# Optimization experiments

Measured on AMD Instinct MI355X. Metric: run time of the kernel, lower is better.

## Reference

```python
import jax, jax.numpy as jnp
import numpy as np

V_MIN = -10.0
V_MAX = 10.0
N_ATOMS = 101
LN_EPS = 1e-5

B = 131072
N_OBS = 60
N_ACT = 20
H = 256


def _layer_norm(x, g, b):
    mu = jnp.mean(x, axis=-1, keepdims=True)
    var = jnp.mean(jnp.square(x - mu), axis=-1, keepdims=True)
    return (x - mu) * jax.lax.rsqrt(var + LN_EPS) * g + b


def _mlp(x, W1, b1, g1, be1, W2, b2, g2, be2, W3, b3, g3, be3, W4, b4):
    h = jax.nn.silu(_layer_norm(x @ W1 + b1, g1, be1))
    h = jax.nn.silu(_layer_norm(h @ W2 + b2, g2, be2))
    h = jax.nn.silu(_layer_norm(h @ W3 + b3, g3, be3))
    return h @ W4 + b4  # [B, N_ATOMS] logits


def setup_inputs() -> dict:
    key = jax.random.key(0)
    ks = jax.random.split(key, 10)
    s = 0.05
    return {
        'obs': jax.random.normal(ks[0], (B, N_OBS), jnp.float32),
        'actions': jax.random.normal(ks[1], (B, N_ACT), jnp.float32),
        'rewards': jax.random.normal(ks[2], (B,), jnp.float32),
        'bootstrap': jax.random.uniform(ks[3], (B,), jnp.float32),
        'discount': jax.random.uniform(ks[4], (B,), jnp.float32, 0.95, 0.99),
        'q_support': jnp.linspace(V_MIN, V_MAX, N_ATOMS, dtype=jnp.float32),
        'W1': jax.random.normal(ks[5], (N_OBS + N_ACT, H), jnp.float32) * s,
        'b1': jnp.zeros((H,), jnp.float32),
        'g1': jnp.ones((H,), jnp.float32),
        'be1': jnp.zeros((H,), jnp.float32),
        'W2': jax.random.normal(ks[6], (H, H // 2), jnp.float32) * s,
        'b2': jnp.zeros((H // 2,), jnp.float32),
        'g2': jnp.ones((H // 2,), jnp.float32),
        'be2': jnp.zeros((H // 2,), jnp.float32),
        'W3': jax.random.normal(ks[7], (H // 2, H // 4), jnp.float32) * s,
        'b3': jnp.zeros((H // 4,), jnp.float32),
        'g3': jnp.ones((H // 4,), jnp.float32),
        'be3': jnp.zeros((H // 4,), jnp.float32),
        'W4': jax.random.normal(ks[8], (H // 4, N_ATOMS), jnp.float32) * s,
        'b4': jnp.zeros((N_ATOMS,), jnp.float32),
    }


def reference(obs, actions, rewards, bootstrap, discount, q_support,
              W1, b1, g1, be1, W2, b2, g2, be2, W3, b3, g3, be3, W4, b4):
    batch = rewards.shape[0]
    delta_z = (V_MAX - V_MIN) / (N_ATOMS - 1)
    # Bellman target support: [B, N_ATOMS]
    target_z = rewards[:, None] + bootstrap[:, None] * discount[:, None] * q_support
    target_z = jnp.clip(target_z, V_MIN, V_MAX)
    b = (target_z - V_MIN) / delta_z
    li = jnp.floor(b).astype(jnp.int32)
    ui = jnp.ceil(b).astype(jnp.int32)
    is_int = ui == li
    lower_mask = is_int & (li > 0)
    upper_mask = is_int & (li == 0)
    li = jnp.where(lower_mask, li - 1, li)
    ui = jnp.where(upper_mask, ui + 1, ui)
    lf = li.astype(b.dtype)
    uf = ui.astype(b.dtype)

    x = jnp.concatenate([obs, actions], axis=-1)
    logits = _mlp(x, W1, b1, g1, be1, W2, b2, g2, be2, W3, b3, g3, be3, W4, b4)
    next_dist = jax.nn.softmax(logits, axis=1)

    size = batch * N_ATOMS
    offset = (jnp.arange(batch, dtype=jnp.int32) * N_ATOMS)[:, None]
    l_idx = jnp.clip((li + offset).reshape(-1), 0, size - 1)
    u_idx = jnp.clip((ui + offset).reshape(-1), 0, size - 1)
    lw = (next_dist * (uf - b)).reshape(-1)
    uw = (next_dist * (b - lf)).reshape(-1)
    proj = jnp.zeros((size,), next_dist.dtype).at[l_idx].add(lw).at[u_idx].add(uw)
    return proj.reshape(batch, N_ATOMS)
```

## Files before the change

kernel.cpp:

```cpp
#include <hip/hip_runtime.h>
#include <math.h>

typedef __bf16 bf16x8 __attribute__((ext_vector_type(8)));
typedef float f32x4 __attribute__((ext_vector_type(4)));

__global__ void conv_weights(const float* __restrict__ W1, const float* __restrict__ W2,
                             const float* __restrict__ W3, const float* __restrict__ W4,
                             __bf16* __restrict__ ws)
{
  const int f = blockIdx.x * 4 + (threadIdx.x >> 6);
  const int lane = threadIdx.x & 63;
  int f0, ntot, Ksrc, Nsrc, off;
  const float* W;
  if (f < 48)       { f0 = f;       ntot = 16; Ksrc = 80;  Nsrc = 256; W = W1; off = 0; }
  else if (f < 112) { f0 = f - 48;  ntot = 8;  Ksrc = 256; Nsrc = 128; W = W2; off = 24576; }
  else if (f < 128) { f0 = f - 112; ntot = 4;  Ksrc = 128; Nsrc = 64;  W = W3; off = 57344; }
  else              { f0 = f - 128; ntot = 8;  Ksrc = 64;  Nsrc = 101; W = W4; off = 65536; }
  const int kt = f0 / ntot, nt = f0 % ntot;
  const int q = lane >> 4, c = lane & 15;
  const int n = nt * 16 + c;
  bf16x8 v;
#pragma unroll
  for (int j = 0; j < 8; ++j) {
    const int k = kt * 32 + q * 8 + j;
    const float x = (k < Ksrc && n < Nsrc) ? W[k * Nsrc + n] : 0.f;
    v[j] = (__bf16)x;
  }
  ((bf16x8*)(ws + off))[f0 * 64 + lane] = v;
}


__global__ __launch_bounds__(256, 3)
void sacq_wave(const float* __restrict__ obs,  const float* __restrict__ act,
               const float* __restrict__ rew,  const float* __restrict__ boot,
               const float* __restrict__ disc, const float* __restrict__ qsup,
               const float* __restrict__ b1, const float* __restrict__ g1, const float* __restrict__ be1,
               const float* __restrict__ b2, const float* __restrict__ g2, const float* __restrict__ be2,
               const float* __restrict__ b3, const float* __restrict__ g3, const float* __restrict__ be3,
               const float* __restrict__ b4,
               const __bf16* __restrict__ ws,
               float* __restrict__ out)
{
  __shared__ float sm[13120];
  const int t = threadIdx.x;
  const int wv = t >> 6, lane = t & 63;
  const int q = lane >> 4, c = lane & 15;
  float* smw = sm + wv * 3280;
  __bf16* h1 = (__bf16*)smw;
  __bf16* h2 = (__bf16*)(smw + 2192);
  __bf16* h3 = (__bf16*)smw;
  float*  proj = smw + 576;
  const int row0w = blockIdx.x * 64 + wv * 16;
  const bf16x8* wsf = (const bf16x8*)ws;

  f32x4 acc1[16];
  {
    bf16x8 A1[3];
    const float4* ob4 = (const float4*)(obs + (size_t)(row0w + c) * 60);
    const float4* ac4 = (const float4*)(act + (size_t)(row0w + c) * 20);
#pragma unroll
    for (int kt = 0; kt < 3; ++kt) {
      const int k0 = kt * 32 + q * 8;
      float v[8];
      if (k0 < 56) {
        const float4 a = ob4[k0 / 4], b = ob4[k0 / 4 + 1];
        v[0]=a.x; v[1]=a.y; v[2]=a.z; v[3]=a.w; v[4]=b.x; v[5]=b.y; v[6]=b.z; v[7]=b.w;
      } else if (k0 == 56) {
        const float4 a = ob4[14], b = ac4[0];
        v[0]=a.x; v[1]=a.y; v[2]=a.z; v[3]=a.w; v[4]=b.x; v[5]=b.y; v[6]=b.z; v[7]=b.w;
      } else if (k0 < 80) {
        const float4 a = ac4[(k0 - 60) / 4], b = ac4[(k0 - 60) / 4 + 1];
        v[0]=a.x; v[1]=a.y; v[2]=a.z; v[3]=a.w; v[4]=b.x; v[5]=b.y; v[6]=b.z; v[7]=b.w;
      } else {
#pragma unroll
        for (int j = 0; j < 8; ++j) v[j] = 0.f;
      }
#pragma unroll
      for (int j = 0; j < 8; ++j) A1[kt][j] = (__bf16)v[j];
    }
#pragma unroll
    for (int nt = 0; nt < 16; ++nt) {
      const float bb = b1[nt * 16 + c];
      f32x4 vv = {bb, bb, bb, bb};
      acc1[nt] = vv;
    }
#pragma unroll
    for (int ch = 0; ch < 4; ++ch) {
      bf16x8 Bb[3][4];
#pragma unroll
      for (int kt = 0; kt < 3; ++kt)
#pragma unroll
        for (int j = 0; j < 4; ++j)
          Bb[kt][j] = wsf[(kt * 16 + ch * 4 + j) * 64 + lane];
#pragma unroll
      for (int kt = 0; kt < 3; ++kt)
#pragma unroll
        for (int j = 0; j < 4; ++j)
          acc1[ch * 4 + j] = __builtin_amdgcn_mfma_f32_16x16x32_bf16(A1[kt], Bb[kt][j], acc1[ch * 4 + j], 0, 0, 0);
    }
    float mu[4], rs[4];
#pragma unroll
    for (int r = 0; r < 4; ++r) {
      float s = 0.f, s2 = 0.f;
#pragma unroll
      for (int nt = 0; nt < 16; ++nt) { const float v = acc1[nt][r]; s += v; s2 += v * v; }
      s += __shfl_xor(s, 1); s2 += __shfl_xor(s2, 1);
      s += __shfl_xor(s, 2); s2 += __shfl_xor(s2, 2);
      s += __shfl_xor(s, 4); s2 += __shfl_xor(s2, 4);
      s += __shfl_xor(s, 8); s2 += __shfl_xor(s2, 8);
      const float m = s * (1.f / 256.f);
      mu[r] = m;
      rs[r] = rsqrtf(s2 * (1.f / 256.f) - m * m + 1e-5f);
    }
#pragma unroll
    for (int nt = 0; nt < 16; ++nt) {
      const int col = nt * 16 + c;
      const float gg = g1[col], bb = be1[col];
#pragma unroll
      for (int r = 0; r < 4; ++r) {
        float v = (acc1[nt][r] - mu[r]) * rs[r] * gg + bb;
        v = v * __builtin_amdgcn_rcpf(1.f + __expf(-v));
        h1[(4 * q + r) * 264 + col] = (__bf16)v;
      }
    }
  }

  {
    f32x4 acc2[8];
#pragma unroll
    for (int nt = 0; nt < 8; ++nt) {
      const float bb = b2[nt * 16 + c];
      f32x4 vv = {bb, bb, bb, bb};
      acc2[nt] = vv;
    }
    bf16x8 B2[3][8];
#pragma unroll
    for (int nt = 0; nt < 8; ++nt) B2[0][nt] = wsf[3072 + (0 * 8 + nt) * 64 + lane];
#pragma unroll
    for (int nt = 0; nt < 8; ++nt) B2[1][nt] = wsf[3072 + (1 * 8 + nt) * 64 + lane];
#pragma unroll
    for (int kt = 0; kt < 8; ++kt) {
      if (kt + 2 < 8) {
#pragma unroll
        for (int nt = 0; nt < 8; ++nt)
          B2[(kt + 2) % 3][nt] = wsf[3072 + ((kt + 2) * 8 + nt) * 64 + lane];
      }
      const bf16x8 A2 = *(const bf16x8*)(h1 + c * 264 + kt * 32 + q * 8);
#pragma unroll
      for (int nt = 0; nt < 8; ++nt)
        acc2[nt] = __builtin_amdgcn_mfma_f32_16x16x32_bf16(A2, B2[kt % 3][nt], acc2[nt], 0, 0, 0);
    }
    float mu[4], rs[4];
#pragma unroll
    for (int r = 0; r < 4; ++r) {
      float s = 0.f, s2 = 0.f;
#pragma unroll
      for (int nt = 0; nt < 8; ++nt) { const float v = acc2[nt][r]; s += v; s2 += v * v; }
      s += __shfl_xor(s, 1); s2 += __shfl_xor(s2, 1);
      s += __shfl_xor(s, 2); s2 += __shfl_xor(s2, 2);
      s += __shfl_xor(s, 4); s2 += __shfl_xor(s2, 4);
      s += __shfl_xor(s, 8); s2 += __shfl_xor(s2, 8);
      const float m = s * (1.f / 128.f);
      mu[r] = m;
      rs[r] = rsqrtf(s2 * (1.f / 128.f) - m * m + 1e-5f);
    }
#pragma unroll
    for (int nt = 0; nt < 8; ++nt) {
      const int col = nt * 16 + c;
      const float gg = g2[col], bb = be2[col];
#pragma unroll
      for (int r = 0; r < 4; ++r) {
        float v = (acc2[nt][r] - mu[r]) * rs[r] * gg + bb;
        v = v * __builtin_amdgcn_rcpf(1.f + __expf(-v));
        h2[(4 * q + r) * 136 + col] = (__bf16)v;
      }
    }
  }

  {
    bf16x8 B3[4][4];
#pragma unroll
    for (int kt = 0; kt < 4; ++kt)
#pragma unroll
      for (int nt = 0; nt < 4; ++nt)
        B3[kt][nt] = wsf[7168 + (kt * 4 + nt) * 64 + lane];
    f32x4 acc3[4];
#pragma unroll
    for (int nt = 0; nt < 4; ++nt) {
      const float bb = b3[nt * 16 + c];
      f32x4 vv = {bb, bb, bb, bb};
      acc3[nt] = vv;
    }
#pragma unroll
    for (int kt = 0; kt < 4; ++kt) {
      const bf16x8 A3 = *(const bf16x8*)(h2 + c * 136 + kt * 32 + q * 8);
#pragma unroll
      for (int nt = 0; nt < 4; ++nt)
        acc3[nt] = __builtin_amdgcn_mfma_f32_16x16x32_bf16(A3, B3[kt][nt], acc3[nt], 0, 0, 0);
    }
    float mu[4], rs[4];
#pragma unroll
    for (int r = 0; r < 4; ++r) {
      float s = 0.f, s2 = 0.f;
#pragma unroll
      for (int nt = 0; nt < 4; ++nt) { const float v = acc3[nt][r]; s += v; s2 += v * v; }
      s += __shfl_xor(s, 1); s2 += __shfl_xor(s2, 1);
      s += __shfl_xor(s, 2); s2 += __shfl_xor(s2, 2);
      s += __shfl_xor(s, 4); s2 += __shfl_xor(s2, 4);
      s += __shfl_xor(s, 8); s2 += __shfl_xor(s2, 8);
      const float m = s * (1.f / 64.f);
      mu[r] = m;
      rs[r] = rsqrtf(s2 * (1.f / 64.f) - m * m + 1e-5f);
    }
#pragma unroll
    for (int nt = 0; nt < 4; ++nt) {
      const int col = nt * 16 + c;
      const float gg = g3[col], bb = be3[col];
#pragma unroll
      for (int r = 0; r < 4; ++r) {
        float v = (acc3[nt][r] - mu[r]) * rs[r] * gg + bb;
        v = v * __builtin_amdgcn_rcpf(1.f + __expf(-v));
        h3[(4 * q + r) * 72 + col] = (__bf16)v;
      }
    }
  }

  {
    bf16x8 B4[2][7];
#pragma unroll
    for (int kt = 0; kt < 2; ++kt)
#pragma unroll
      for (int nt = 0; nt < 7; ++nt)
        B4[kt][nt] = wsf[8192 + (kt * 8 + nt) * 64 + lane];
    f32x4 a4[7];
#pragma unroll
    for (int nt = 0; nt < 7; ++nt) {
      const int col = nt * 16 + c;
      const float bb = (col < 101) ? b4[col] : 0.f;
      f32x4 vv = {bb, bb, bb, bb};
      a4[nt] = vv;
    }
#pragma unroll
    for (int kt = 0; kt < 2; ++kt) {
      const bf16x8 A4 = *(const bf16x8*)(h3 + c * 72 + kt * 32 + q * 8);
#pragma unroll
      for (int nt = 0; nt < 7; ++nt)
        a4[nt] = __builtin_amdgcn_mfma_f32_16x16x32_bf16(A4, B4[kt][nt], a4[nt], 0, 0, 0);
    }

    {
      f32x4 z = {0.f, 0.f, 0.f, 0.f};
      f32x4* p4 = (f32x4*)proj;
      for (int i = lane; i < 404; i += 64) p4[i] = z;
    }

    float mx4[4] = {-3.4e38f, -3.4e38f, -3.4e38f, -3.4e38f};
#pragma unroll
    for (int nt = 0; nt < 7; ++nt) {
      const bool ok = (nt < 6) | (c < 5);
#pragma unroll
      for (int r = 0; r < 4; ++r)
        if (ok) mx4[r] = fmaxf(mx4[r], a4[nt][r]);
    }
#pragma unroll
    for (int r = 0; r < 4; ++r) {
      mx4[r] = fmaxf(mx4[r], __shfl_xor(mx4[r], 1));
      mx4[r] = fmaxf(mx4[r], __shfl_xor(mx4[r], 2));
      mx4[r] = fmaxf(mx4[r], __shfl_xor(mx4[r], 4));
      mx4[r] = fmaxf(mx4[r], __shfl_xor(mx4[r], 8));
    }
    float sm4[4] = {0.f, 0.f, 0.f, 0.f};
#pragma unroll
    for (int nt = 0; nt < 7; ++nt) {
      const bool ok = (nt < 6) | (c < 5);
#pragma unroll
      for (int r = 0; r < 4; ++r) {
        const float e = ok ? __expf(a4[nt][r] - mx4[r]) : 0.f;
        a4[nt][r] = e;
        sm4[r] += e;
      }
    }
    float inv4[4];
#pragma unroll
    for (int r = 0; r < 4; ++r) {
      float s = sm4[r];
      s += __shfl_xor(s, 1);
      s += __shfl_xor(s, 2);
      s += __shfl_xor(s, 4);
      s += __shfl_xor(s, 8);
      inv4[r] = __builtin_amdgcn_rcpf(s);
    }

    float rwv[4], bdv[4];
#pragma unroll
    for (int r = 0; r < 4; ++r) {
      const int gr = row0w + 4 * q + r;
      rwv[r] = rew[gr];
      bdv[r] = boot[gr] * disc[gr];
    }

#pragma unroll
    for (int nt = 0; nt < 7; ++nt) {
      const int col = nt * 16 + c;
      if ((nt < 6) | (c < 5)) {
        const float qsv = qsup[col];
#pragma unroll
        for (int r = 0; r < 4; ++r) {
          const float p = a4[nt][r] * inv4[r];
          float tz = rwv[r] + bdv[r] * qsv;
          tz = fminf(fmaxf(tz, -10.f), 10.f);
          const float b_ = (tz + 10.f) * 5.f;
          const float fl = floorf(b_), cl = ceilf(b_);
          int li = (int)fl, ui = (int)cl;
          if (ui == li) { if (li > 0) --li; else ++ui; }
          const int rb = (4 * q + r) * 101;
          atomicAdd(&proj[rb + li], p * ((float)ui - b_));
          atomicAdd(&proj[rb + ui], p * (b_ - (float)li));
        }
      }
    }
  }

  {
    const f32x4* p4 = (const f32x4*)proj;
    f32x4* o4 = (f32x4*)(out + (size_t)row0w * 101);
    for (int i = lane; i < 404; i += 64) o4[i] = p4[i];
  }
}

extern "C" void kernel_launch(void* const* d_in, const int* in_sizes, int n_in,
                              void* d_out, int out_size, void* d_ws, size_t ws_size,
                              hipStream_t stream)
{
  const int B = in_sizes[2];
  __bf16* ws = (__bf16*)d_ws;

  conv_weights<<<dim3(36), dim3(256), 0, stream>>>(
      (const float*)d_in[6], (const float*)d_in[10], (const float*)d_in[14],
      (const float*)d_in[18], ws);

  sacq_wave<<<dim3(B / 64), dim3(256), 0, stream>>>(
      (const float*)d_in[0],  (const float*)d_in[1],  (const float*)d_in[2],
      (const float*)d_in[3],  (const float*)d_in[4],  (const float*)d_in[5],
      (const float*)d_in[7],  (const float*)d_in[8],  (const float*)d_in[9],
      (const float*)d_in[11], (const float*)d_in[12], (const float*)d_in[13],
      (const float*)d_in[15], (const float*)d_in[16], (const float*)d_in[17],
      (const float*)d_in[19], ws, (float*)d_out);
}
```

Baseline: 329.5 us.

## Split fused MLP into two kernels staging weight fragments in LDS

When the workspace is large enough, the single fused kernel is replaced by two kernels. The first computes layers 1–2, staging bf16 weight fragments through shared memory in chunks, and writes h2 to a global buffer in MFMA fragment layout. The second stages the W3/W4 fragments once per block, processes two tiles per wave, and does layer 3, layer 4, softmax and the distributional projection. This is meant to replace repeated per-wave global weight-fragment loads with shared-memory reuse. It adds an extra global round trip for the h2 activations (about 32 MB written and read) and extra block barriers; the fallback kernel is also simplified by dropping its weight prefetch.

```diff
diff --git a/kernel.cpp b/kernel.cpp
--- a/kernel.cpp
+++ b/kernel.cpp
@@ -29,6 +29,337 @@
   ((bf16x8*)(ws + off))[f0 * 64 + lane] = v;
 }
 
+__device__ __forceinline__ void stage_frags(const __bf16* __restrict__ ws,
+                                            __bf16* __restrict__ wbuf,
+                                            int f0, int nf, int t)
+{
+  const uint4* __restrict__ src = (const uint4*)(ws + (size_t)f0 * 512);
+  uint4* __restrict__ dst = (uint4*)wbuf;
+  const int cnt = nf * 64;
+  for (int i = t; i < cnt; i += 256) dst[i] = src[i];
+}
+
+__device__ __forceinline__ bf16x8 wfrag(const __bf16* __restrict__ wbuf, int slot, int lane)
+{
+  return *(const bf16x8*)(wbuf + slot * 512 + lane * 8);
+}
+
+__global__ __launch_bounds__(256, 2)
+void k12(const float* __restrict__ obs, const float* __restrict__ act,
+         const float* __restrict__ b1, const float* __restrict__ g1, const float* __restrict__ be1,
+         const float* __restrict__ b2, const float* __restrict__ g2, const float* __restrict__ be2,
+         const __bf16* __restrict__ ws, __bf16* __restrict__ h2f)
+{
+  __shared__ __bf16 wbuf[16384];
+  __shared__ __bf16 h1s[4][16 * 264];
+  const int t = threadIdx.x;
+  const int wv = t >> 6, lane = t & 63;
+  const int q = lane >> 4, c = lane & 15;
+  const int tile = blockIdx.x * 4 + wv;
+  const int row0w = tile * 16;
+  __bf16* h1 = &h1s[wv][0];
+
+  bf16x8 A1[3];
+  {
+    const float4* ob4 = (const float4*)(obs + (size_t)(row0w + c) * 60);
+    const float4* ac4 = (const float4*)(act + (size_t)(row0w + c) * 20);
+#pragma unroll
+    for (int kt = 0; kt < 3; ++kt) {
+      const int k0 = kt * 32 + q * 8;
+      float v[8];
+      if (k0 < 56) {
+        const float4 a = ob4[k0 / 4], b = ob4[k0 / 4 + 1];
+        v[0]=a.x; v[1]=a.y; v[2]=a.z; v[3]=a.w; v[4]=b.x; v[5]=b.y; v[6]=b.z; v[7]=b.w;
+      } else if (k0 == 56) {
+        const float4 a = ob4[14], b = ac4[0];
+        v[0]=a.x; v[1]=a.y; v[2]=a.z; v[3]=a.w; v[4]=b.x; v[5]=b.y; v[6]=b.z; v[7]=b.w;
+      } else if (k0 < 80) {
+        const float4 a = ac4[(k0 - 60) / 4], b = ac4[(k0 - 60) / 4 + 1];
+        v[0]=a.x; v[1]=a.y; v[2]=a.z; v[3]=a.w; v[4]=b.x; v[5]=b.y; v[6]=b.z; v[7]=b.w;
+      } else {
+#pragma unroll
+        for (int j = 0; j < 8; ++j) v[j] = 0.f;
+      }
+#pragma unroll
+      for (int j = 0; j < 8; ++j) A1[kt][j] = (__bf16)v[j];
+    }
+  }
+
+  f32x4 acc1[16];
+#pragma unroll
+  for (int nt = 0; nt < 16; ++nt) {
+    const float bb = b1[nt * 16 + c];
+    f32x4 vv = {bb, bb, bb, bb};
+    acc1[nt] = vv;
+  }
+  stage_frags(ws, wbuf, 0, 32, t);
+  __syncthreads();
+#pragma unroll
+  for (int kt = 0; kt < 2; ++kt)
+#pragma unroll
+    for (int nt = 0; nt < 16; ++nt)
+      acc1[nt] = __builtin_amdgcn_mfma_f32_16x16x32_bf16(A1[kt], wfrag(wbuf, kt * 16 + nt, lane), acc1[nt], 0, 0, 0);
+  __syncthreads();
+  stage_frags(ws, wbuf, 32, 16, t);
+  __syncthreads();
+#pragma unroll
+  for (int nt = 0; nt < 16; ++nt)
+    acc1[nt] = __builtin_amdgcn_mfma_f32_16x16x32_bf16(A1[2], wfrag(wbuf, nt, lane), acc1[nt], 0, 0, 0);
+
+  {
+    float mu[4], rs[4];
+#pragma unroll
+    for (int r = 0; r < 4; ++r) {
+      float s = 0.f, s2 = 0.f;
+#pragma unroll
+      for (int nt = 0; nt < 16; ++nt) { const float v = acc1[nt][r]; s += v; s2 += v * v; }
+      s += __shfl_xor(s, 1); s2 += __shfl_xor(s2, 1);
+      s += __shfl_xor(s, 2); s2 += __shfl_xor(s2, 2);
+      s += __shfl_xor(s, 4); s2 += __shfl_xor(s2, 4);
+      s += __shfl_xor(s, 8); s2 += __shfl_xor(s2, 8);
+      const float m = s * (1.f / 256.f);
+      mu[r] = m;
+      rs[r] = rsqrtf(s2 * (1.f / 256.f) - m * m + 1e-5f);
+    }
+#pragma unroll
+    for (int nt = 0; nt < 16; ++nt) {
+      const int col = nt * 16 + c;
+      const float gg = g1[col], bb = be1[col];
+#pragma unroll
+      for (int r = 0; r < 4; ++r) {
+        float v = (acc1[nt][r] - mu[r]) * rs[r] * gg + bb;
+        v = v * __builtin_amdgcn_rcpf(1.f + __expf(-v));
+        h1[(4 * q + r) * 264 + col] = (__bf16)v;
+      }
+    }
+  }
+  __syncthreads();
+
+  f32x4 acc2[8];
+#pragma unroll
+  for (int nt = 0; nt < 8; ++nt) {
+    const float bb = b2[nt * 16 + c];
+    f32x4 vv = {bb, bb, bb, bb};
+    acc2[nt] = vv;
+  }
+  stage_frags(ws, wbuf, 48, 32, t);
+  __syncthreads();
+#pragma unroll
+  for (int kt = 0; kt < 4; ++kt) {
+    const bf16x8 A2 = *(const bf16x8*)(h1 + c * 264 + kt * 32 + q * 8);
+#pragma unroll
+    for (int nt = 0; nt < 8; ++nt)
+      acc2[nt] = __builtin_amdgcn_mfma_f32_16x16x32_bf16(A2, wfrag(wbuf, kt * 8 + nt, lane), acc2[nt], 0, 0, 0);
+  }
+  __syncthreads();
+  stage_frags(ws, wbuf, 80, 32, t);
+  __syncthreads();
+#pragma unroll
+  for (int kt = 4; kt < 8; ++kt) {
+    const bf16x8 A2 = *(const bf16x8*)(h1 + c * 264 + kt * 32 + q * 8);
+#pragma unroll
+    for (int nt = 0; nt < 8; ++nt)
+      acc2[nt] = __builtin_amdgcn_mfma_f32_16x16x32_bf16(A2, wfrag(wbuf, (kt - 4) * 8 + nt, lane), acc2[nt], 0, 0, 0);
+  }
+
+  {
+    float mu[4], rs[4];
+#pragma unroll
+    for (int r = 0; r < 4; ++r) {
+      float s = 0.f, s2 = 0.f;
+#pragma unroll
+      for (int nt = 0; nt < 8; ++nt) { const float v = acc2[nt][r]; s += v; s2 += v * v; }
+      s += __shfl_xor(s, 1); s2 += __shfl_xor(s2, 1);
+      s += __shfl_xor(s, 2); s2 += __shfl_xor(s2, 2);
+      s += __shfl_xor(s, 4); s2 += __shfl_xor(s2, 4);
+      s += __shfl_xor(s, 8); s2 += __shfl_xor(s2, 8);
+      const float m = s * (1.f / 128.f);
+      mu[r] = m;
+      rs[r] = rsqrtf(s2 * (1.f / 128.f) - m * m + 1e-5f);
+    }
+    __bf16* hs = h1;
+#pragma unroll
+    for (int nt = 0; nt < 8; ++nt) {
+      const int col = nt * 16 + c;
+      const float gg = g2[col], bb = be2[col];
+#pragma unroll
+      for (int r = 0; r < 4; ++r) {
+        float v = (acc2[nt][r] - mu[r]) * rs[r] * gg + bb;
+        v = v * __builtin_amdgcn_rcpf(1.f + __expf(-v));
+        hs[(4 * q + r) * 136 + col] = (__bf16)v;
+      }
+    }
+#pragma unroll
+    for (int kt = 0; kt < 4; ++kt) {
+      const bf16x8 v = *(const bf16x8*)(hs + c * 136 + kt * 32 + q * 8);
+      *(bf16x8*)(h2f + ((size_t)(tile * 4 + kt) * 64 + lane) * 8) = v;
+    }
+  }
+}
+
+__global__ __launch_bounds__(256, 2)
+void k34(const float* __restrict__ rew, const float* __restrict__ boot,
+         const float* __restrict__ disc, const float* __restrict__ qsup,
+         const float* __restrict__ b3, const float* __restrict__ g3, const float* __restrict__ be3,
+         const float* __restrict__ b4,
+         const __bf16* __restrict__ ws, const __bf16* __restrict__ h2f,
+         float* __restrict__ out)
+{
+  __shared__ __bf16 wbuf[16384];
+  __shared__ float pws[4][2192];
+  const int t = threadIdx.x;
+  const int wv = t >> 6, lane = t & 63;
+  const int q = lane >> 4, c = lane & 15;
+  __bf16* h3 = (__bf16*)&pws[wv][0];
+  float* proj = &pws[wv][576];
+
+  stage_frags(ws, wbuf, 112, 32, t);
+  __syncthreads();
+
+  for (int s = 0; s < 2; ++s) {
+    const int tile = blockIdx.x * 8 + wv * 2 + s;
+    const int row0w = tile * 16;
+
+    bf16x8 A3[4];
+#pragma unroll
+    for (int kt = 0; kt < 4; ++kt)
+      A3[kt] = *(const bf16x8*)(h2f + ((size_t)(tile * 4 + kt) * 64 + lane) * 8);
+
+    f32x4 acc3[4];
+#pragma unroll
+    for (int nt = 0; nt < 4; ++nt) {
+      const float bb = b3[nt * 16 + c];
+      f32x4 vv = {bb, bb, bb, bb};
+      acc3[nt] = vv;
+    }
+#pragma unroll
+    for (int kt = 0; kt < 4; ++kt)
+#pragma unroll
+      for (int nt = 0; nt < 4; ++nt)
+        acc3[nt] = __builtin_amdgcn_mfma_f32_16x16x32_bf16(A3[kt], wfrag(wbuf, kt * 4 + nt, lane), acc3[nt], 0, 0, 0);
+    {
+      float mu[4], rs[4];
+#pragma unroll
+      for (int r = 0; r < 4; ++r) {
+        float ss = 0.f, s2 = 0.f;
+#pragma unroll
+        for (int nt = 0; nt < 4; ++nt) { const float v = acc3[nt][r]; ss += v; s2 += v * v; }
+        ss += __shfl_xor(ss, 1); s2 += __shfl_xor(s2, 1);
+        ss += __shfl_xor(ss, 2); s2 += __shfl_xor(s2, 2);
+        ss += __shfl_xor(ss, 4); s2 += __shfl_xor(s2, 4);
+        ss += __shfl_xor(ss, 8); s2 += __shfl_xor(s2, 8);
+        const float m = ss * (1.f / 64.f);
+        mu[r] = m;
+        rs[r] = rsqrtf(s2 * (1.f / 64.f) - m * m + 1e-5f);
+      }
+#pragma unroll
+      for (int nt = 0; nt < 4; ++nt) {
+        const int col = nt * 16 + c;
+        const float gg = g3[col], bb = be3[col];
+#pragma unroll
+        for (int r = 0; r < 4; ++r) {
+          float v = (acc3[nt][r] - mu[r]) * rs[r] * gg + bb;
+          v = v * __builtin_amdgcn_rcpf(1.f + __expf(-v));
+          h3[(4 * q + r) * 72 + col] = (__bf16)v;
+        }
+      }
+    }
+
+    f32x4 a4[7];
+#pragma unroll
+    for (int nt = 0; nt < 7; ++nt) {
+      const int col = nt * 16 + c;
+      const float bb = (col < 101) ? b4[col] : 0.f;
+      f32x4 vv = {bb, bb, bb, bb};
+      a4[nt] = vv;
+    }
+#pragma unroll
+    for (int kt = 0; kt < 2; ++kt) {
+      const bf16x8 A4 = *(const bf16x8*)(h3 + c * 72 + kt * 32 + q * 8);
+#pragma unroll
+      for (int nt = 0; nt < 7; ++nt)
+        a4[nt] = __builtin_amdgcn_mfma_f32_16x16x32_bf16(A4, wfrag(wbuf, 16 + kt * 8 + nt, lane), a4[nt], 0, 0, 0);
+    }
+
+    {
+      f32x4 z = {0.f, 0.f, 0.f, 0.f};
+      f32x4* p4 = (f32x4*)proj;
+      for (int i = lane; i < 404; i += 64) p4[i] = z;
+    }
+
+    float mx4[4] = {-3.4e38f, -3.4e38f, -3.4e38f, -3.4e38f};
+#pragma unroll
+    for (int nt = 0; nt < 7; ++nt) {
+      const bool ok = (nt < 6) | (c < 5);
+#pragma unroll
+      for (int r = 0; r < 4; ++r)
+        if (ok) mx4[r] = fmaxf(mx4[r], a4[nt][r]);
+    }
+#pragma unroll
+    for (int r = 0; r < 4; ++r) {
+      mx4[r] = fmaxf(mx4[r], __shfl_xor(mx4[r], 1));
+      mx4[r] = fmaxf(mx4[r], __shfl_xor(mx4[r], 2));
+      mx4[r] = fmaxf(mx4[r], __shfl_xor(mx4[r], 4));
+      mx4[r] = fmaxf(mx4[r], __shfl_xor(mx4[r], 8));
+    }
+    float sm4[4] = {0.f, 0.f, 0.f, 0.f};
+#pragma unroll
+    for (int nt = 0; nt < 7; ++nt) {
+      const bool ok = (nt < 6) | (c < 5);
+#pragma unroll
+      for (int r = 0; r < 4; ++r) {
+        const float e = ok ? __expf(a4[nt][r] - mx4[r]) : 0.f;
+        a4[nt][r] = e;
+        sm4[r] += e;
+      }
+    }
+    float inv4[4];
+#pragma unroll
+    for (int r = 0; r < 4; ++r) {
+      float ss = sm4[r];
+      ss += __shfl_xor(ss, 1);
+      ss += __shfl_xor(ss, 2);
+      ss += __shfl_xor(ss, 4);
+      ss += __shfl_xor(ss, 8);
+      inv4[r] = __builtin_amdgcn_rcpf(ss);
+    }
+
+    float rwv[4], bdv[4];
+#pragma unroll
+    for (int r = 0; r < 4; ++r) {
+      const int gr = row0w + 4 * q + r;
+      rwv[r] = rew[gr];
+      bdv[r] = boot[gr] * disc[gr];
+    }
+
+#pragma unroll
+    for (int nt = 0; nt < 7; ++nt) {
+      const int col = nt * 16 + c;
+      if ((nt < 6) | (c < 5)) {
+        const float qsv = qsup[col];
+#pragma unroll
+        for (int r = 0; r < 4; ++r) {
+          const float p = a4[nt][r] * inv4[r];
+          float tz = rwv[r] + bdv[r] * qsv;
+          tz = fminf(fmaxf(tz, -10.f), 10.f);
+          const float b_ = (tz + 10.f) * 5.f;
+          const float fl = floorf(b_), cl = ceilf(b_);
+          int li = (int)fl, ui = (int)cl;
+          if (ui == li) { if (li > 0) --li; else ++ui; }
+          const int rb = (4 * q + r) * 101;
+          atomicAdd(&proj[rb + li], p * ((float)ui - b_));
+          atomicAdd(&proj[rb + ui], p * (b_ - (float)li));
+        }
+      }
+    }
+
+    {
+      const f32x4* p4 = (const f32x4*)proj;
+      f32x4* o4 = (f32x4*)(out + (size_t)row0w * 101);
+      for (int i = lane; i < 404; i += 64) o4[i] = p4[i];
+    }
+  }
+}
 
 __global__ __launch_bounds__(256, 3)
 void sacq_wave(const float* __restrict__ obs,  const float* __restrict__ act,
@@ -53,51 +384,34 @@
   const int row0w = blockIdx.x * 64 + wv * 16;
   const bf16x8* wsf = (const bf16x8*)ws;
 
+  bf16x8 A1[3];
+  {
+    const float* obsR = obs + (size_t)(row0w + c) * 60;
+    const float* actR = act + (size_t)(row0w + c) * 20;
+#pragma unroll
+    for (int kt = 0; kt < 3; ++kt)
+#pragma unroll
+      for (int j = 0; j < 8; ++j) {
+        const int k = kt * 32 + q * 8 + j;
+        float xv = 0.f;
+        if (k < 60) xv = obsR[k];
+        else if (k < 80) xv = actR[k - 60];
+        A1[kt][j] = (__bf16)xv;
+      }
+  }
   f32x4 acc1[16];
-  {
-    bf16x8 A1[3];
-    const float4* ob4 = (const float4*)(obs + (size_t)(row0w + c) * 60);
-    const float4* ac4 = (const float4*)(act + (size_t)(row0w + c) * 20);
-#pragma unroll
-    for (int kt = 0; kt < 3; ++kt) {
-      const int k0 = kt * 32 + q * 8;
-      float v[8];
-      if (k0 < 56) {
-        const float4 a = ob4[k0 / 4], b = ob4[k0 / 4 + 1];
-        v[0]=a.x; v[1]=a.y; v[2]=a.z; v[3]=a.w; v[4]=b.x; v[5]=b.y; v[6]=b.z; v[7]=b.w;
-      } else if (k0 == 56) {
-        const float4 a = ob4[14], b = ac4[0];
-        v[0]=a.x; v[1]=a.y; v[2]=a.z; v[3]=a.w; v[4]=b.x; v[5]=b.y; v[6]=b.z; v[7]=b.w;
-      } else if (k0 < 80) {
-        const float4 a = ac4[(k0 - 60) / 4], b = ac4[(k0 - 60) / 4 + 1];
-        v[0]=a.x; v[1]=a.y; v[2]=a.z; v[3]=a.w; v[4]=b.x; v[5]=b.y; v[6]=b.z; v[7]=b.w;
-      } else {
-#pragma unroll
-        for (int j = 0; j < 8; ++j) v[j] = 0.f;
-      }
-#pragma unroll
-      for (int j = 0; j < 8; ++j) A1[kt][j] = (__bf16)v[j];
-    }
-#pragma unroll
-    for (int nt = 0; nt < 16; ++nt) {
-      const float bb = b1[nt * 16 + c];
-      f32x4 vv = {bb, bb, bb, bb};
-      acc1[nt] = vv;
-    }
-#pragma unroll
-    for (int ch = 0; ch < 4; ++ch) {
-      bf16x8 Bb[3][4];
-#pragma unroll
-      for (int kt = 0; kt < 3; ++kt)
-#pragma unroll
-        for (int j = 0; j < 4; ++j)
-          Bb[kt][j] = wsf[(kt * 16 + ch * 4 + j) * 64 + lane];
-#pragma unroll
-      for (int kt = 0; kt < 3; ++kt)
-#pragma unroll
-        for (int j = 0; j < 4; ++j)
-          acc1[ch * 4 + j] = __builtin_amdgcn_mfma_f32_16x16x32_bf16(A1[kt], Bb[kt][j], acc1[ch * 4 + j], 0, 0, 0);
-    }
+#pragma unroll
+  for (int nt = 0; nt < 16; ++nt) {
+    const float bb = b1[nt * 16 + c];
+    f32x4 vv = {bb, bb, bb, bb};
+    acc1[nt] = vv;
+  }
+#pragma unroll
+  for (int kt = 0; kt < 3; ++kt)
+#pragma unroll
+    for (int nt = 0; nt < 16; ++nt)
+      acc1[nt] = __builtin_amdgcn_mfma_f32_16x16x32_bf16(A1[kt], wsf[(kt * 16 + nt) * 64 + lane], acc1[nt], 0, 0, 0);
+  {
     float mu[4], rs[4];
 #pragma unroll
     for (int r = 0; r < 4; ++r) {
@@ -124,7 +438,6 @@
       }
     }
   }
-
   {
     f32x4 acc2[8];
 #pragma unroll
@@ -133,22 +446,12 @@
       f32x4 vv = {bb, bb, bb, bb};
       acc2[nt] = vv;
     }
-    bf16x8 B2[3][8];
-#pragma unroll
-    for (int nt = 0; nt < 8; ++nt) B2[0][nt] = wsf[3072 + (0 * 8 + nt) * 64 + lane];
-#pragma unroll
-    for (int nt = 0; nt < 8; ++nt) B2[1][nt] = wsf[3072 + (1 * 8 + nt) * 64 + lane];
 #pragma unroll
     for (int kt = 0; kt < 8; ++kt) {
-      if (kt + 2 < 8) {
-#pragma unroll
-        for (int nt = 0; nt < 8; ++nt)
-          B2[(kt + 2) % 3][nt] = wsf[3072 + ((kt + 2) * 8 + nt) * 64 + lane];
-      }
       const bf16x8 A2 = *(const bf16x8*)(h1 + c * 264 + kt * 32 + q * 8);
 #pragma unroll
       for (int nt = 0; nt < 8; ++nt)
-        acc2[nt] = __builtin_amdgcn_mfma_f32_16x16x32_bf16(A2, B2[kt % 3][nt], acc2[nt], 0, 0, 0);
+        acc2[nt] = __builtin_amdgcn_mfma_f32_16x16x32_bf16(A2, wsf[3072 + (kt * 8 + nt) * 64 + lane], acc2[nt], 0, 0, 0);
     }
     float mu[4], rs[4];
 #pragma unroll
@@ -176,14 +479,7 @@
       }
     }
   }
-
-  {
-    bf16x8 B3[4][4];
-#pragma unroll
-    for (int kt = 0; kt < 4; ++kt)
-#pragma unroll
-      for (int nt = 0; nt < 4; ++nt)
-        B3[kt][nt] = wsf[7168 + (kt * 4 + nt) * 64 + lane];
+  {
     f32x4 acc3[4];
 #pragma unroll
     for (int nt = 0; nt < 4; ++nt) {
@@ -196,7 +492,7 @@
       const bf16x8 A3 = *(const bf16x8*)(h2 + c * 136 + kt * 32 + q * 8);
 #pragma unroll
       for (int nt = 0; nt < 4; ++nt)
-        acc3[nt] = __builtin_amdgcn_mfma_f32_16x16x32_bf16(A3, B3[kt][nt], acc3[nt], 0, 0, 0);
+        acc3[nt] = __builtin_amdgcn_mfma_f32_16x16x32_bf16(A3, wsf[7168 + (kt * 4 + nt) * 64 + lane], acc3[nt], 0, 0, 0);
     }
     float mu[4], rs[4];
 #pragma unroll
@@ -224,14 +520,7 @@
       }
     }
   }
-
-  {
-    bf16x8 B4[2][7];
-#pragma unroll
-    for (int kt = 0; kt < 2; ++kt)
-#pragma unroll
-      for (int nt = 0; nt < 7; ++nt)
-        B4[kt][nt] = wsf[8192 + (kt * 8 + nt) * 64 + lane];
+  {
     f32x4 a4[7];
 #pragma unroll
     for (int nt = 0; nt < 7; ++nt) {
@@ -245,15 +534,13 @@
       const bf16x8 A4 = *(const bf16x8*)(h3 + c * 72 + kt * 32 + q * 8);
 #pragma unroll
       for (int nt = 0; nt < 7; ++nt)
-        a4[nt] = __builtin_amdgcn_mfma_f32_16x16x32_bf16(A4, B4[kt][nt], a4[nt], 0, 0, 0);
-    }
-
+        a4[nt] = __builtin_amdgcn_mfma_f32_16x16x32_bf16(A4, wsf[8192 + (kt * 8 + nt) * 64 + lane], a4[nt], 0, 0, 0);
+    }
     {
       f32x4 z = {0.f, 0.f, 0.f, 0.f};
       f32x4* p4 = (f32x4*)proj;
       for (int i = lane; i < 404; i += 64) p4[i] = z;
     }
-
     float mx4[4] = {-3.4e38f, -3.4e38f, -3.4e38f, -3.4e38f};
 #pragma unroll
     for (int nt = 0; nt < 7; ++nt) {
@@ -290,7 +577,6 @@
       s += __shfl_xor(s, 8);
       inv4[r] = __builtin_amdgcn_rcpf(s);
     }
-
     float rwv[4], bdv[4];
 #pragma unroll
     for (int r = 0; r < 4; ++r) {
@@ -298,7 +584,6 @@
       rwv[r] = rew[gr];
       bdv[r] = boot[gr] * disc[gr];
     }
-
 #pragma unroll
     for (int nt = 0; nt < 7; ++nt) {
       const int col = nt * 16 + c;
@@ -320,7 +605,6 @@
       }
     }
   }
-
   {
     const f32x4* p4 = (const f32x4*)proj;
     f32x4* o4 = (f32x4*)(out + (size_t)row0w * 101);
@@ -334,16 +618,32 @@
 {
   const int B = in_sizes[2];
   __bf16* ws = (__bf16*)d_ws;
+  const size_t needW  = 147456;
+  const size_t needH2 = (size_t)B * 128 * 2;
 
   conv_weights<<<dim3(36), dim3(256), 0, stream>>>(
       (const float*)d_in[6], (const float*)d_in[10], (const float*)d_in[14],
       (const float*)d_in[18], ws);
 
-  sacq_wave<<<dim3(B / 64), dim3(256), 0, stream>>>(
-      (const float*)d_in[0],  (const float*)d_in[1],  (const float*)d_in[2],
-      (const float*)d_in[3],  (const float*)d_in[4],  (const float*)d_in[5],
-      (const float*)d_in[7],  (const float*)d_in[8],  (const float*)d_in[9],
-      (const float*)d_in[11], (const float*)d_in[12], (const float*)d_in[13],
-      (const float*)d_in[15], (const float*)d_in[16], (const float*)d_in[17],
-      (const float*)d_in[19], ws, (float*)d_out);
+  if (ws_size >= needW + needH2) {
+    __bf16* h2f = (__bf16*)((char*)d_ws + needW);
+    k12<<<dim3(B / 64), dim3(256), 0, stream>>>(
+        (const float*)d_in[0], (const float*)d_in[1],
+        (const float*)d_in[7], (const float*)d_in[8], (const float*)d_in[9],
+        (const float*)d_in[11], (const float*)d_in[12], (const float*)d_in[13],
+        ws, h2f);
+    k34<<<dim3(B / 128), dim3(256), 0, stream>>>(
+        (const float*)d_in[2], (const float*)d_in[3], (const float*)d_in[4],
+        (const float*)d_in[5],
+        (const float*)d_in[15], (const float*)d_in[16], (const float*)d_in[17],
+        (const float*)d_in[19], ws, h2f, (float*)d_out);
+  } else {
+    sacq_wave<<<dim3(B / 64), dim3(256), 0, stream>>>(
+        (const float*)d_in[0],  (const float*)d_in[1],  (const float*)d_in[2],
+        (const float*)d_in[3],  (const float*)d_in[4],  (const float*)d_in[5],
+        (const float*)d_in[7],  (const float*)d_in[8],  (const float*)d_in[9],
+        (const float*)d_in[11], (const float*)d_in[12], (const float*)d_in[13],
+        (const float*)d_in[15], (const float*)d_in[16], (const float*)d_in[17],
+        (const float*)d_in[19], ws, (float*)d_out);
+  }
 }
```

Result: slower. 346.9 us (+5.3%).

## Stage weight fragments through double-buffered LDS via global_load_lds

Applied to the files above, without the earlier changes.

Instead of each wave loading its own copy of every bf16 weight fragment from global memory into registers, the block now cooperatively streams 8-fragment chunks into two shared-memory buffers with async global_load_lds, computing on one while filling the other. This cuts redundant global/L2 weight traffic (4x per block) and register pressure from prefetched B fragments. In exchange it adds a block-wide barrier per chunk across all four layers, more LDS use, and lowers the launch-bounds occupancy hint from 3 to 2 blocks per CU.

```diff
diff --git a/kernel.cpp b/kernel.cpp
--- a/kernel.cpp
+++ b/kernel.cpp
@@ -29,33 +29,54 @@
   ((bf16x8*)(ws + off))[f0 * 64 + lane] = v;
 }
 
-
-__global__ __launch_bounds__(256, 3)
-void sacq_wave(const float* __restrict__ obs,  const float* __restrict__ act,
-               const float* __restrict__ rew,  const float* __restrict__ boot,
-               const float* __restrict__ disc, const float* __restrict__ qsup,
-               const float* __restrict__ b1, const float* __restrict__ g1, const float* __restrict__ be1,
-               const float* __restrict__ b2, const float* __restrict__ g2, const float* __restrict__ be2,
-               const float* __restrict__ b3, const float* __restrict__ g3, const float* __restrict__ be3,
-               const float* __restrict__ b4,
-               const __bf16* __restrict__ ws,
-               float* __restrict__ out)
-{
-  __shared__ float sm[13120];
+__device__ __forceinline__ void stage8(const __bf16* __restrict__ ws,
+                                       __bf16* __restrict__ buf,
+                                       int f0, int wv, int lane)
+{
+#pragma unroll
+  for (int i = 0; i < 2; ++i) {
+    const int f = wv * 2 + i;
+    __builtin_amdgcn_global_load_lds(
+        (const __attribute__((address_space(1))) void*)(ws + (size_t)(f0 + f) * 512 + lane * 8),
+        (__attribute__((address_space(3))) void*)(buf + f * 512),
+        16, 0, 0);
+  }
+}
+
+__device__ __forceinline__ bf16x8 wfrag(const __bf16* __restrict__ buf, int slot, int lane)
+{
+  return *(const bf16x8*)(buf + slot * 512 + lane * 8);
+}
+
+
+__global__ __launch_bounds__(256, 2)
+void sacq_fused(const float* __restrict__ obs,  const float* __restrict__ act,
+                const float* __restrict__ rew,  const float* __restrict__ boot,
+                const float* __restrict__ disc, const float* __restrict__ qsup,
+                const float* __restrict__ b1, const float* __restrict__ g1, const float* __restrict__ be1,
+                const float* __restrict__ b2, const float* __restrict__ g2, const float* __restrict__ be2,
+                const float* __restrict__ b3, const float* __restrict__ g3, const float* __restrict__ be3,
+                const float* __restrict__ b4,
+                const __bf16* __restrict__ ws,
+                float* __restrict__ out)
+{
+  __shared__ __bf16 wbufA[4096];
+  __shared__ __bf16 wbufB[4096];
+  __shared__ float acts[4][3280];
   const int t = threadIdx.x;
   const int wv = t >> 6, lane = t & 63;
   const int q = lane >> 4, c = lane & 15;
-  float* smw = sm + wv * 3280;
+  float* smw = &acts[wv][0];
   __bf16* h1 = (__bf16*)smw;
   __bf16* h2 = (__bf16*)(smw + 2192);
   __bf16* h3 = (__bf16*)smw;
   float*  proj = smw + 576;
   const int row0w = blockIdx.x * 64 + wv * 16;
-  const bf16x8* wsf = (const bf16x8*)ws;
-
-  f32x4 acc1[16];
-  {
-    bf16x8 A1[3];
+
+  stage8(ws, wbufA, 0, wv, lane);
+
+  bf16x8 A1[3];
+  {
     const float4* ob4 = (const float4*)(obs + (size_t)(row0w + c) * 60);
     const float4* ac4 = (const float4*)(act + (size_t)(row0w + c) * 20);
 #pragma unroll
@@ -78,26 +99,30 @@
 #pragma unroll
       for (int j = 0; j < 8; ++j) A1[kt][j] = (__bf16)v[j];
     }
-#pragma unroll
-    for (int nt = 0; nt < 16; ++nt) {
-      const float bb = b1[nt * 16 + c];
-      f32x4 vv = {bb, bb, bb, bb};
-      acc1[nt] = vv;
-    }
-#pragma unroll
-    for (int ch = 0; ch < 4; ++ch) {
-      bf16x8 Bb[3][4];
-#pragma unroll
-      for (int kt = 0; kt < 3; ++kt)
-#pragma unroll
-        for (int j = 0; j < 4; ++j)
-          Bb[kt][j] = wsf[(kt * 16 + ch * 4 + j) * 64 + lane];
-#pragma unroll
-      for (int kt = 0; kt < 3; ++kt)
-#pragma unroll
-        for (int j = 0; j < 4; ++j)
-          acc1[ch * 4 + j] = __builtin_amdgcn_mfma_f32_16x16x32_bf16(A1[kt], Bb[kt][j], acc1[ch * 4 + j], 0, 0, 0);
-    }
+  }
+
+  f32x4 acc1[16];
+#pragma unroll
+  for (int nt = 0; nt < 16; ++nt) {
+    const float bb = b1[nt * 16 + c];
+    f32x4 vv = {bb, bb, bb, bb};
+    acc1[nt] = vv;
+  }
+  __syncthreads();
+
+#pragma unroll
+  for (int ci = 0; ci < 6; ++ci) {
+    __bf16* curb = (ci & 1) ? wbufB : wbufA;
+    __bf16* nxtb = (ci & 1) ? wbufA : wbufB;
+    stage8(ws, nxtb, (ci < 5) ? (ci + 1) * 8 : 48, wv, lane);
+    const int kt = ci >> 1, nb = (ci & 1) * 8;
+#pragma unroll
+    for (int j = 0; j < 8; ++j)
+      acc1[nb + j] = __builtin_amdgcn_mfma_f32_16x16x32_bf16(A1[kt], wfrag(curb, j, lane), acc1[nb + j], 0, 0, 0);
+    __syncthreads();
+  }
+
+  {
     float mu[4], rs[4];
 #pragma unroll
     for (int r = 0; r < 4; ++r) {
@@ -125,31 +150,26 @@
     }
   }
 
-  {
-    f32x4 acc2[8];
-#pragma unroll
-    for (int nt = 0; nt < 8; ++nt) {
-      const float bb = b2[nt * 16 + c];
-      f32x4 vv = {bb, bb, bb, bb};
-      acc2[nt] = vv;
-    }
-    bf16x8 B2[3][8];
-#pragma unroll
-    for (int nt = 0; nt < 8; ++nt) B2[0][nt] = wsf[3072 + (0 * 8 + nt) * 64 + lane];
-#pragma unroll
-    for (int nt = 0; nt < 8; ++nt) B2[1][nt] = wsf[3072 + (1 * 8 + nt) * 64 + lane];
-#pragma unroll
-    for (int kt = 0; kt < 8; ++kt) {
-      if (kt + 2 < 8) {
-#pragma unroll
-        for (int nt = 0; nt < 8; ++nt)
-          B2[(kt + 2) % 3][nt] = wsf[3072 + ((kt + 2) * 8 + nt) * 64 + lane];
-      }
-      const bf16x8 A2 = *(const bf16x8*)(h1 + c * 264 + kt * 32 + q * 8);
-#pragma unroll
-      for (int nt = 0; nt < 8; ++nt)
-        acc2[nt] = __builtin_amdgcn_mfma_f32_16x16x32_bf16(A2, B2[kt % 3][nt], acc2[nt], 0, 0, 0);
-    }
+  f32x4 acc2[8];
+#pragma unroll
+  for (int nt = 0; nt < 8; ++nt) {
+    const float bb = b2[nt * 16 + c];
+    f32x4 vv = {bb, bb, bb, bb};
+    acc2[nt] = vv;
+  }
+#pragma unroll
+  for (int kt = 0; kt < 8; ++kt) {
+    __bf16* curb = (kt & 1) ? wbufB : wbufA;
+    __bf16* nxtb = (kt & 1) ? wbufA : wbufB;
+    stage8(ws, nxtb, (kt < 7) ? 48 + (kt + 1) * 8 : 112, wv, lane);
+    const bf16x8 A2 = *(const bf16x8*)(h1 + c * 264 + kt * 32 + q * 8);
+#pragma unroll
+    for (int nt = 0; nt < 8; ++nt)
+      acc2[nt] = __builtin_amdgcn_mfma_f32_16x16x32_bf16(A2, wfrag(curb, nt, lane), acc2[nt], 0, 0, 0);
+    __syncthreads();
+  }
+
+  {
     float mu[4], rs[4];
 #pragma unroll
     for (int r = 0; r < 4; ++r) {
@@ -177,27 +197,30 @@
     }
   }
 
-  {
-    bf16x8 B3[4][4];
-#pragma unroll
-    for (int kt = 0; kt < 4; ++kt)
+  f32x4 acc3[4];
+#pragma unroll
+  for (int nt = 0; nt < 4; ++nt) {
+    const float bb = b3[nt * 16 + c];
+    f32x4 vv = {bb, bb, bb, bb};
+    acc3[nt] = vv;
+  }
+#pragma unroll
+  for (int cc = 0; cc < 2; ++cc) {
+    __bf16* curb = (cc & 1) ? wbufB : wbufA;
+    __bf16* nxtb = (cc & 1) ? wbufA : wbufB;
+    stage8(ws, nxtb, (cc == 0) ? 120 : 128, wv, lane);
+#pragma unroll
+    for (int k2 = 0; k2 < 2; ++k2) {
+      const int kt = cc * 2 + k2;
+      const bf16x8 A3 = *(const bf16x8*)(h2 + c * 136 + kt * 32 + q * 8);
 #pragma unroll
       for (int nt = 0; nt < 4; ++nt)
-        B3[kt][nt] = wsf[7168 + (kt * 4 + nt) * 64 + lane];
-    f32x4 acc3[4];
-#pragma unroll
-    for (int nt = 0; nt < 4; ++nt) {
-      const float bb = b3[nt * 16 + c];
-      f32x4 vv = {bb, bb, bb, bb};
-      acc3[nt] = vv;
-    }
-#pragma unroll
-    for (int kt = 0; kt < 4; ++kt) {
-      const bf16x8 A3 = *(const bf16x8*)(h2 + c * 136 + kt * 32 + q * 8);
-#pragma unroll
-      for (int nt = 0; nt < 4; ++nt)
-        acc3[nt] = __builtin_amdgcn_mfma_f32_16x16x32_bf16(A3, B3[kt][nt], acc3[nt], 0, 0, 0);
-    }
+        acc3[nt] = __builtin_amdgcn_mfma_f32_16x16x32_bf16(A3, wfrag(curb, k2 * 4 + nt, lane), acc3[nt], 0, 0, 0);
+    }
+    __syncthreads();
+  }
+
+  {
     float mu[4], rs[4];
 #pragma unroll
     for (int r = 0; r < 4; ++r) {
@@ -225,35 +248,31 @@
     }
   }
 
-  {
-    bf16x8 B4[2][7];
-#pragma unroll
-    for (int kt = 0; kt < 2; ++kt)
-#pragma unroll
-      for (int nt = 0; nt < 7; ++nt)
-        B4[kt][nt] = wsf[8192 + (kt * 8 + nt) * 64 + lane];
-    f32x4 a4[7];
-#pragma unroll
-    for (int nt = 0; nt < 7; ++nt) {
-      const int col = nt * 16 + c;
-      const float bb = (col < 101) ? b4[col] : 0.f;
-      f32x4 vv = {bb, bb, bb, bb};
-      a4[nt] = vv;
-    }
-#pragma unroll
-    for (int kt = 0; kt < 2; ++kt) {
-      const bf16x8 A4 = *(const bf16x8*)(h3 + c * 72 + kt * 32 + q * 8);
-#pragma unroll
-      for (int nt = 0; nt < 7; ++nt)
-        a4[nt] = __builtin_amdgcn_mfma_f32_16x16x32_bf16(A4, B4[kt][nt], a4[nt], 0, 0, 0);
-    }
-
+  f32x4 a4[7];
+#pragma unroll
+  for (int nt = 0; nt < 7; ++nt) {
+    const int col = nt * 16 + c;
+    const float bb = (col < 101) ? b4[col] : 0.f;
+    f32x4 vv = {bb, bb, bb, bb};
+    a4[nt] = vv;
+  }
+#pragma unroll
+  for (int kt = 0; kt < 2; ++kt) {
+    __bf16* curb = kt ? wbufB : wbufA;
+    if (kt == 0) stage8(ws, wbufB, 136, wv, lane);
+    const bf16x8 A4 = *(const bf16x8*)(h3 + c * 72 + kt * 32 + q * 8);
+#pragma unroll
+    for (int nt = 0; nt < 7; ++nt)
+      a4[nt] = __builtin_amdgcn_mfma_f32_16x16x32_bf16(A4, wfrag(curb, nt, lane), a4[nt], 0, 0, 0);
+    __syncthreads();
+  }
+
+  {
     {
       f32x4 z = {0.f, 0.f, 0.f, 0.f};
       f32x4* p4 = (f32x4*)proj;
       for (int i = lane; i < 404; i += 64) p4[i] = z;
     }
-
     float mx4[4] = {-3.4e38f, -3.4e38f, -3.4e38f, -3.4e38f};
 #pragma unroll
     for (int nt = 0; nt < 7; ++nt) {
@@ -290,7 +309,6 @@
       s += __shfl_xor(s, 8);
       inv4[r] = __builtin_amdgcn_rcpf(s);
     }
-
     float rwv[4], bdv[4];
 #pragma unroll
     for (int r = 0; r < 4; ++r) {
@@ -298,7 +316,6 @@
       rwv[r] = rew[gr];
       bdv[r] = boot[gr] * disc[gr];
     }
-
 #pragma unroll
     for (int nt = 0; nt < 7; ++nt) {
       const int col = nt * 16 + c;
@@ -339,7 +356,7 @@
       (const float*)d_in[6], (const float*)d_in[10], (const float*)d_in[14],
       (const float*)d_in[18], ws);
 
-  sacq_wave<<<dim3(B / 64), dim3(256), 0, stream>>>(
+  sacq_fused<<<dim3(B / 64), dim3(256), 0, stream>>>(
       (const float*)d_in[0],  (const float*)d_in[1],  (const float*)d_in[2],
       (const float*)d_in[3],  (const float*)d_in[4],  (const float*)d_in[5],
       (const float*)d_in[7],  (const float*)d_in[8],  (const float*)d_in[9],
```

Result: slower. 336.9 us (+2.2%).
